# Optimization experiments

Measured on AMD Instinct MI355X. Metric: run time of the kernel, lower is better.

## Reference

```python
import jax, jax.numpy as jnp
import numpy as np

PADDED_NODE_ID = -1


def setup_inputs() -> dict:
    key = jax.random.key(0)
    k0, k1, k2, k3 = jax.random.split(key, 4)
    B, N, F = 1024, 512, 64
    src_ids = jax.random.randint(k0, (B, N), 0, 1000, dtype=jnp.int64 if jax.config.jax_enable_x64 else jnp.int32)
    dst_ids = jax.random.randint(k1, (B, N), 0, 1000, dtype=src_ids.dtype)
    W1 = jax.random.normal(k2, (1, F), dtype=jnp.float32) * 0.1   # Linear(1 -> F)
    b1 = jnp.zeros((F,), dtype=jnp.float32)
    W2 = jax.random.normal(k3, (F, F), dtype=jnp.float32) * 0.05  # Linear(F -> F)
    b2 = jnp.zeros((F,), dtype=jnp.float32)
    return {"src_ids": src_ids, "dst_ids": dst_ids, "W1": W1, "b1": b1, "W2": W2, "b2": b2}


def _count_freqs(src_ids, dst_ids):
    # For each row, count occurrences of each neighbor id within its own row
    # and within the paired row (cross-lookup). Equivalent to np.unique counts
    # plus dict-based cross mapping in the original, vectorized as pairwise
    # equality reductions over [B, N, N].
    def eq_count(a, b):
        return (a[:, :, None] == b[:, None, :]).sum(-1).astype(jnp.float32)  # [B, N]

    src_in_src = eq_count(src_ids, src_ids)
    src_in_dst = eq_count(src_ids, dst_ids)
    dst_in_dst = eq_count(dst_ids, dst_ids)
    dst_in_src = eq_count(dst_ids, src_ids)

    source_freq = jnp.stack([src_in_src, src_in_dst], axis=-1)  # [B, N, 2]
    dst_freq = jnp.stack([dst_in_dst, dst_in_src], axis=-1)     # [B, N, 2]

    # zero out padded positions
    source_freq = jnp.where((src_ids == PADDED_NODE_ID)[..., None], 0.0, source_freq)
    dst_freq = jnp.where((dst_ids == PADDED_NODE_ID)[..., None], 0.0, dst_freq)
    return source_freq, dst_freq


def reference(src_ids, dst_ids, W1, b1, W2, b2):
    source_freq, dst_freq = _count_freqs(src_ids, dst_ids)  # [B, N, 2] each

    def encode(freq):
        # freq[..., None] has shape [B, N, 2, 1]; Linear(1->F) is an outer product
        h = jax.nn.relu(freq[..., None] * W1[0] + b1)        # [B, N, 2, F]
        h = jnp.einsum('bnkf,fg->bnkg', h, W2) + b2          # [B, N, 2, F]
        return h.sum(axis=2)                                 # [B, N, F]

    return encode(source_freq), encode(dst_freq)
```

## Files before the change

kernel.cpp:

```cpp
#include <hip/hip_runtime.h>

#define BATCH 1024
#define NSEQ  512
#define NF    64
#define TBL_N (NSEQ + 1)
#define HIST_BINS 1024

__global__ void build_table_kernel(const float* __restrict__ W1,
                                   const float* __restrict__ b1,
                                   const float* __restrict__ W2,
                                   const float* __restrict__ b2,
                                   float* __restrict__ tbl) {
    const int c = blockIdx.x;
    const int g = threadIdx.x;
    const float cf = (float)c;
    float acc = b2[g];
#pragma unroll 8
    for (int f = 0; f < NF; ++f) {
        float h = fmaxf(cf * W1[f] + b1[f], 0.0f);
        acc += h * W2[f * NF + g];
    }
    tbl[c * NF + g] = acc;
}

__global__ __launch_bounds__(256) void cooc_encode_kernel(
        const int* __restrict__ src_ids,
        const int* __restrict__ dst_ids,
        const float* __restrict__ tbl,
        float* __restrict__ out_src,
        float* __restrict__ out_dst) {
    __shared__ int s_src[NSEQ];
    __shared__ int s_dst[NSEQ];
    __shared__ int hist_s[HIST_BINS];
    __shared__ int hist_d[HIST_BINS];
    __shared__ int c_ss[NSEQ], c_sd[NSEQ], c_dd[NSEQ], c_ds[NSEQ];

    const int b = blockIdx.x;
    const int t = threadIdx.x;

#pragma unroll
    for (int i = t; i < HIST_BINS; i += 256) { hist_s[i] = 0; hist_d[i] = 0; }
#pragma unroll
    for (int i = t; i < NSEQ; i += 256) {
        s_src[i] = src_ids[(size_t)b * NSEQ + i];
        s_dst[i] = dst_ids[(size_t)b * NSEQ + i];
    }
    __syncthreads();

#pragma unroll
    for (int i = t; i < NSEQ; i += 256) {
        int si = s_src[i], di = s_dst[i];
        if (si >= 0) atomicAdd(&hist_s[si], 1);
        if (di >= 0) atomicAdd(&hist_d[di], 1);
    }
    __syncthreads();

#pragma unroll
    for (int i = t; i < NSEQ; i += 256) {
        int si = s_src[i], di = s_dst[i];
        c_ss[i] = (si >= 0) ? hist_s[si] : 0;
        c_sd[i] = (si >= 0) ? hist_d[si] : 0;
        c_dd[i] = (di >= 0) ? hist_d[di] : 0;
        c_ds[i] = (di >= 0) ? hist_s[di] : 0;
    }
    __syncthreads();

    const float4* __restrict__ tbl4 = (const float4*)tbl;
    float4* __restrict__ o0 = (float4*)(out_src + (size_t)b * NSEQ * NF);
    float4* __restrict__ o1 = (float4*)(out_dst + (size_t)b * NSEQ * NF);
    const int NV = NSEQ * NF / 4;
#pragma unroll 4
    for (int e = t; e < NV; e += 256) {
        int n  = e >> 4;
        int f4 = e & 15;
        float4 a0 = tbl4[c_ss[n] * (NF / 4) + f4];
        float4 a1 = tbl4[c_sd[n] * (NF / 4) + f4];
        o0[e] = make_float4(a0.x + a1.x, a0.y + a1.y, a0.z + a1.z, a0.w + a1.w);
        float4 d0 = tbl4[c_dd[n] * (NF / 4) + f4];
        float4 d1 = tbl4[c_ds[n] * (NF / 4) + f4];
        o1[e] = make_float4(d0.x + d1.x, d0.y + d1.y, d0.z + d1.z, d0.w + d1.w);
    }
}

extern "C" void kernel_launch(void* const* d_in, const int* in_sizes, int n_in,
                              void* d_out, int out_size, void* d_ws, size_t ws_size,
                              hipStream_t stream) {
    const int*   src_ids = (const int*)d_in[0];
    const int*   dst_ids = (const int*)d_in[1];
    const float* W1 = (const float*)d_in[2];
    const float* b1 = (const float*)d_in[3];
    const float* W2 = (const float*)d_in[4];
    const float* b2 = (const float*)d_in[5];

    float* out_src = (float*)d_out;
    float* out_dst = (float*)d_out + (size_t)BATCH * NSEQ * NF;

    float* tbl = (float*)d_ws;

    build_table_kernel<<<TBL_N, NF, 0, stream>>>(W1, b1, W2, b2, tbl);
    cooc_encode_kernel<<<BATCH, 256, 0, stream>>>(src_ids, dst_ids, tbl,
                                                  out_src, out_dst);
}
```

Before: 52.01 us.

## Split counting and output expansion into separate kernels with nontemporal stores

Splits the fused per-row kernel into a count kernel, which writes packed ushort4 co-occurrence counts to workspace, and a grid-stride expand kernel. The expand kernel gathers table rows and writes outputs with nontemporal stores. The goal is to decouple the store-bound expansion from the histogram phase's shared-memory use and barriers so it gets better occupancy and streaming stores. The cost is an extra launch and a round trip of the counts through memory. The fused kernel remains as a fallback when the workspace is too small.

```diff
diff --git a/kernel.cpp b/kernel.cpp
--- a/kernel.cpp
+++ b/kernel.cpp
@@ -5,6 +5,8 @@
 #define NF    64
 #define TBL_N (NSEQ + 1)
 #define HIST_BINS 1024
+
+typedef float f32x4 __attribute__((ext_vector_type(4)));
 
 __global__ void build_table_kernel(const float* __restrict__ W1,
                                    const float* __restrict__ b1,
@@ -21,6 +23,70 @@
         acc += h * W2[f * NF + g];
     }
     tbl[c * NF + g] = acc;
+}
+
+__global__ __launch_bounds__(256) void count_kernel(
+        const int* __restrict__ src_ids,
+        const int* __restrict__ dst_ids,
+        ushort4* __restrict__ counts) {
+    __shared__ int s_src[NSEQ];
+    __shared__ int s_dst[NSEQ];
+    __shared__ int hist_s[HIST_BINS];
+    __shared__ int hist_d[HIST_BINS];
+
+    const int b = blockIdx.x;
+    const int t = threadIdx.x;
+
+#pragma unroll
+    for (int i = t; i < HIST_BINS; i += 256) { hist_s[i] = 0; hist_d[i] = 0; }
+#pragma unroll
+    for (int i = t; i < NSEQ; i += 256) {
+        s_src[i] = src_ids[(size_t)b * NSEQ + i];
+        s_dst[i] = dst_ids[(size_t)b * NSEQ + i];
+    }
+    __syncthreads();
+
+#pragma unroll
+    for (int i = t; i < NSEQ; i += 256) {
+        int si = s_src[i], di = s_dst[i];
+        if (si >= 0) atomicAdd(&hist_s[si], 1);
+        if (di >= 0) atomicAdd(&hist_d[di], 1);
+    }
+    __syncthreads();
+
+#pragma unroll
+    for (int i = t; i < NSEQ; i += 256) {
+        int si = s_src[i], di = s_dst[i];
+        ushort4 p;
+        p.x = (si >= 0) ? (unsigned short)hist_s[si] : 0;
+        p.y = (si >= 0) ? (unsigned short)hist_d[si] : 0;
+        p.z = (di >= 0) ? (unsigned short)hist_d[di] : 0;
+        p.w = (di >= 0) ? (unsigned short)hist_s[di] : 0;
+        counts[(size_t)b * NSEQ + i] = p;
+    }
+}
+
+__global__ __launch_bounds__(256) void expand_kernel(
+        const ushort4* __restrict__ counts,
+        const float* __restrict__ tbl,
+        float* __restrict__ out_src,
+        float* __restrict__ out_dst) {
+    const f32x4* __restrict__ tbl4 = (const f32x4*)tbl;
+    f32x4* __restrict__ o0 = (f32x4*)out_src;
+    f32x4* __restrict__ o1 = (f32x4*)out_dst;
+    const long total  = (long)BATCH * NSEQ * (NF / 4);
+    const long stride = (long)gridDim.x * blockDim.x;
+    for (long e = (long)blockIdx.x * blockDim.x + threadIdx.x; e < total; e += stride) {
+        const long n  = e >> 4;
+        const int  f4 = (int)(e & 15);
+        const ushort4 c = counts[n];
+        f32x4 a0 = tbl4[(int)c.x * (NF / 4) + f4];
+        f32x4 a1 = tbl4[(int)c.y * (NF / 4) + f4];
+        __builtin_nontemporal_store(a0 + a1, &o0[e]);
+        f32x4 d0 = tbl4[(int)c.z * (NF / 4) + f4];
+        f32x4 d1 = tbl4[(int)c.w * (NF / 4) + f4];
+        __builtin_nontemporal_store(d0 + d1, &o1[e]);
+    }
 }
 
 __global__ __launch_bounds__(256) void cooc_encode_kernel(
@@ -46,7 +112,6 @@
         s_dst[i] = dst_ids[(size_t)b * NSEQ + i];
     }
     __syncthreads();
-
 #pragma unroll
     for (int i = t; i < NSEQ; i += 256) {
         int si = s_src[i], di = s_dst[i];
@@ -54,7 +119,6 @@
         if (di >= 0) atomicAdd(&hist_d[di], 1);
     }
     __syncthreads();
-
 #pragma unroll
     for (int i = t; i < NSEQ; i += 256) {
         int si = s_src[i], di = s_dst[i];
@@ -95,9 +159,20 @@
     float* out_src = (float*)d_out;
     float* out_dst = (float*)d_out + (size_t)BATCH * NSEQ * NF;
 
+    const size_t tbl_bytes    = (size_t)TBL_N * NF * sizeof(float);
+    const size_t counts_off   = (tbl_bytes + 255) & ~(size_t)255;
+    const size_t counts_bytes = (size_t)BATCH * NSEQ * sizeof(ushort4);
+
     float* tbl = (float*)d_ws;
 
     build_table_kernel<<<TBL_N, NF, 0, stream>>>(W1, b1, W2, b2, tbl);
-    cooc_encode_kernel<<<BATCH, 256, 0, stream>>>(src_ids, dst_ids, tbl,
-                                                  out_src, out_dst);
+
+    if (ws_size >= counts_off + counts_bytes) {
+        ushort4* counts = (ushort4*)((char*)d_ws + counts_off);
+        count_kernel<<<BATCH, 256, 0, stream>>>(src_ids, dst_ids, counts);
+        expand_kernel<<<2048, 256, 0, stream>>>(counts, tbl, out_src, out_dst);
+    } else {
+        cooc_encode_kernel<<<BATCH, 256, 0, stream>>>(src_ids, dst_ids, tbl,
+                                                      out_src, out_dst);
+    }
 }
```

Result: slower. 63.04 us (+21.2%).

## Split encode work into per-row src/dst blocks and pack counts as ushort2

Applied to the files above, without the earlier changes.

The encode kernel now launches two blocks per batch row, one for the source output and one for the destination output, which doubles the grid to improve occupancy and latency hiding on the write-bound expansion. Each block still builds both histograms, so the histogram work is duplicated. Counts are packed into ushort2 in shared memory, and the table-build kernel packs four table rows per 256-thread block.

```diff
diff --git a/kernel.cpp b/kernel.cpp
--- a/kernel.cpp
+++ b/kernel.cpp
@@ -6,13 +6,17 @@
 #define TBL_N (NSEQ + 1)
 #define HIST_BINS 1024
 
-__global__ void build_table_kernel(const float* __restrict__ W1,
-                                   const float* __restrict__ b1,
-                                   const float* __restrict__ W2,
-                                   const float* __restrict__ b2,
-                                   float* __restrict__ tbl) {
-    const int c = blockIdx.x;
-    const int g = threadIdx.x;
+#define TBL_BLOCKS ((TBL_N + 3) / 4)
+
+__global__ __launch_bounds__(256) void build_table_kernel(
+        const float* __restrict__ W1,
+        const float* __restrict__ b1,
+        const float* __restrict__ W2,
+        const float* __restrict__ b2,
+        float* __restrict__ tbl) {
+    const int c = blockIdx.x * 4 + (threadIdx.x >> 6);
+    const int g = threadIdx.x & 63;
+    if (c >= TBL_N) return;
     const float cf = (float)c;
     float acc = b2[g];
 #pragma unroll 8
@@ -23,27 +27,27 @@
     tbl[c * NF + g] = acc;
 }
 
-__global__ __launch_bounds__(256) void cooc_encode_kernel(
+__global__ __launch_bounds__(256) void expand_kernel(
         const int* __restrict__ src_ids,
         const int* __restrict__ dst_ids,
         const float* __restrict__ tbl,
-        float* __restrict__ out_src,
-        float* __restrict__ out_dst) {
-    __shared__ int s_src[NSEQ];
-    __shared__ int s_dst[NSEQ];
-    __shared__ int hist_s[HIST_BINS];
-    __shared__ int hist_d[HIST_BINS];
-    __shared__ int c_ss[NSEQ], c_sd[NSEQ], c_dd[NSEQ], c_ds[NSEQ];
+        float* __restrict__ out) {
+    __shared__ int     s_src[NSEQ];
+    __shared__ int     s_dst[NSEQ];
+    __shared__ int     hist_s[HIST_BINS];
+    __shared__ int     hist_d[HIST_BINS];
+    __shared__ ushort2 s_cnt[NSEQ];
 
-    const int b = blockIdx.x;
-    const int t = threadIdx.x;
+    const int t     = threadIdx.x;
+    const int which = blockIdx.x & 1;
+    const int row   = blockIdx.x >> 1;
 
 #pragma unroll
     for (int i = t; i < HIST_BINS; i += 256) { hist_s[i] = 0; hist_d[i] = 0; }
 #pragma unroll
     for (int i = t; i < NSEQ; i += 256) {
-        s_src[i] = src_ids[(size_t)b * NSEQ + i];
-        s_dst[i] = dst_ids[(size_t)b * NSEQ + i];
+        s_src[i] = src_ids[(size_t)row * NSEQ + i];
+        s_dst[i] = dst_ids[(size_t)row * NSEQ + i];
     }
     __syncthreads();
 
@@ -57,28 +61,29 @@
 
 #pragma unroll
     for (int i = t; i < NSEQ; i += 256) {
-        int si = s_src[i], di = s_dst[i];
-        c_ss[i] = (si >= 0) ? hist_s[si] : 0;
-        c_sd[i] = (si >= 0) ? hist_d[si] : 0;
-        c_dd[i] = (di >= 0) ? hist_d[di] : 0;
-        c_ds[i] = (di >= 0) ? hist_s[di] : 0;
+        int id = (which == 0) ? s_src[i] : s_dst[i];
+        ushort2 c;
+        if (id >= 0) {
+            c.x = (unsigned short)((which == 0) ? hist_s[id] : hist_d[id]);
+            c.y = (unsigned short)((which == 0) ? hist_d[id] : hist_s[id]);
+        } else {
+            c.x = 0; c.y = 0;
+        }
+        s_cnt[i] = c;
     }
     __syncthreads();
 
     const float4* __restrict__ tbl4 = (const float4*)tbl;
-    float4* __restrict__ o0 = (float4*)(out_src + (size_t)b * NSEQ * NF);
-    float4* __restrict__ o1 = (float4*)(out_dst + (size_t)b * NSEQ * NF);
+    float4* __restrict__ o = (float4*)(out + ((size_t)which * BATCH + row) * NSEQ * NF);
     const int NV = NSEQ * NF / 4;
-#pragma unroll 4
+#pragma unroll 8
     for (int e = t; e < NV; e += 256) {
         int n  = e >> 4;
         int f4 = e & 15;
-        float4 a0 = tbl4[c_ss[n] * (NF / 4) + f4];
-        float4 a1 = tbl4[c_sd[n] * (NF / 4) + f4];
-        o0[e] = make_float4(a0.x + a1.x, a0.y + a1.y, a0.z + a1.z, a0.w + a1.w);
-        float4 d0 = tbl4[c_dd[n] * (NF / 4) + f4];
-        float4 d1 = tbl4[c_ds[n] * (NF / 4) + f4];
-        o1[e] = make_float4(d0.x + d1.x, d0.y + d1.y, d0.z + d1.z, d0.w + d1.w);
+        ushort2 c = s_cnt[n];
+        float4 a0 = tbl4[((int)c.x << 4) + f4];
+        float4 a1 = tbl4[((int)c.y << 4) + f4];
+        o[e] = make_float4(a0.x + a1.x, a0.y + a1.y, a0.z + a1.z, a0.w + a1.w);
     }
 }
 
@@ -92,12 +97,9 @@
     const float* W2 = (const float*)d_in[4];
     const float* b2 = (const float*)d_in[5];
 
-    float* out_src = (float*)d_out;
-    float* out_dst = (float*)d_out + (size_t)BATCH * NSEQ * NF;
-
+    float* out = (float*)d_out;
     float* tbl = (float*)d_ws;
 
-    build_table_kernel<<<TBL_N, NF, 0, stream>>>(W1, b1, W2, b2, tbl);
-    cooc_encode_kernel<<<BATCH, 256, 0, stream>>>(src_ids, dst_ids, tbl,
-                                                  out_src, out_dst);
+    build_table_kernel<<<TBL_BLOCKS, 256, 0, stream>>>(W1, b1, W2, b2, tbl);
+    expand_kernel<<<2 * BATCH, 256, 0, stream>>>(src_ids, dst_ids, tbl, out);
 }
```

New measurement: 51.32 us. Within noise of the previous version (-1.3%).
